# Kernel optimization log

Hardware: AMD Instinct MI355X
Metric: run time of the kernel (lower is better)

The kernel has to match this reference:

```python
import jax, jax.numpy as jnp
import numpy as np

STEPS = 2
P_TOPP = 0.9
TAU = 1.0
LN_EPS = 1e-5


def _top_p_attention(pooled, W1, W2, W3):
    # pooled: (N, C). Bilinear scores -> softmax -> nucleus (top-p) sparsify -> renorm.
    e1 = pooled @ W1.T                      # (N, d)
    e3 = pooled @ W3.T                      # (N, d)
    logits = (e1 @ W2.T) @ e3.T / TAU       # (N, N)
    attn = jax.nn.softmax(logits, axis=-1)
    srt = jnp.sort(attn, axis=-1)[:, ::-1]  # descending
    csum = jnp.cumsum(srt, axis=-1)
    keep = (csum - srt) < P_TOPP            # keep entries whose exclusive cum-prob < p
    thr = jnp.min(jnp.where(keep, srt, jnp.inf), axis=-1, keepdims=True)
    masked = jnp.where(attn >= thr, attn, 0.0)
    return masked / jnp.clip(jnp.sum(masked, axis=-1, keepdims=True), 1e-12)


def _layernorm(h, gamma, beta):
    mu = jnp.mean(h, axis=-1, keepdims=True)
    var = jnp.mean(jnp.square(h - mu), axis=-1, keepdims=True)
    return (h - mu) * jax.lax.rsqrt(var + LN_EPS) * gamma + beta


def _forward(x, prior, W1, W2, W3, prior_fwd_w, adaptive_w, ln_gamma, ln_beta, alpha):
    # Row-normalised prior (forward diffusion operator)
    Rf = prior / jnp.clip(jnp.sum(prior, axis=1, keepdims=True), 1e-12)
    Xf = x
    Xa = x
    residual = jnp.zeros_like(x)
    for idx in range(STEPS):
        pooled = jnp.mean(Xa, axis=1)                      # protein axis pooling -> (N_P, C)
        attn = _top_p_attention(pooled, W1, W2, W3)        # (N_P, N_P)
        Xf = jnp.einsum('ij,jkc->ikc', Rf, Xf)
        Xa = jnp.einsum('ij,jkc->ikc', attn, Xa)
        delta = jnp.einsum('ikc,dc->ikd', Xf, prior_fwd_w[idx]) \
              + jnp.einsum('ikc,dc->ikd', Xa, adaptive_w[idx])
        residual = residual + delta                        # dropout is identity in eval mode
    gate = jax.nn.sigmoid(alpha)                           # (1,)
    return _layernorm(x + gate * residual, ln_gamma, ln_beta)


def setup_inputs() -> dict:
    key = jax.random.key(0)
    ks = jax.random.split(key, 8)
    N_P, N_C, C, D = 2048, 64, 128, 64
    x = jax.random.normal(ks[0], (N_P, N_C, C), dtype=jnp.float32)
    prior = jax.random.uniform(ks[1], (N_P, N_P), dtype=jnp.float32)
    W1 = jax.random.normal(ks[2], (D, C), dtype=jnp.float32) / np.sqrt(C)
    W2 = jax.random.normal(ks[3], (D, D), dtype=jnp.float32) / np.sqrt(D)
    W3 = jax.random.normal(ks[4], (D, C), dtype=jnp.float32) / np.sqrt(C)
    prior_fwd_w = jax.random.normal(ks[5], (STEPS, C, C), dtype=jnp.float32) / np.sqrt(C)
    adaptive_w = jax.random.normal(ks[6], (STEPS, C, C), dtype=jnp.float32) / np.sqrt(C)
    ln_gamma = jnp.ones((C,), dtype=jnp.float32)
    ln_beta = jnp.zeros((C,), dtype=jnp.float32)
    alpha = jnp.zeros((1,), dtype=jnp.float32)
    return {"x": x, "prior": prior, "W1": W1, "W2": W2, "W3": W3,
            "prior_fwd_w": prior_fwd_w, "adaptive_w": adaptive_w,
            "ln_gamma": ln_gamma, "ln_beta": ln_beta, "alpha": alpha}


def reference(x, prior, W1, W2, W3, prior_fwd_w, adaptive_w, ln_gamma, ln_beta, alpha):
    return _forward(x, prior, W1, W2, W3, prior_fwd_w, adaptive_w, ln_gamma, ln_beta, alpha)
```

## Files before the change

kernel.cpp:

```cpp
#include <hip/hip_runtime.h>

typedef unsigned short u16;
typedef __attribute__((ext_vector_type(8))) short short8;
typedef __attribute__((ext_vector_type(4))) float f32x4;
typedef __attribute__((ext_vector_type(16))) float f32x16;

#define AS1 __attribute__((address_space(1)))
#define AS3 __attribute__((address_space(3)))

__device__ __forceinline__ void async_cp16(const void* g, void* l) {
  __builtin_amdgcn_global_load_lds((const AS1 unsigned int*)g, (AS3 unsigned int*)l, 16, 0, 0);
}

__device__ __forceinline__ u16 f2bf(float f) {
  union { float f; unsigned u; } v; v.f = f;
  unsigned r = v.u + 0x7fffu + ((v.u >> 16) & 1u);
  return (u16)(r >> 16);
}
__device__ __forceinline__ float bf2f(u16 h) {
  union { unsigned u; float f; } v; v.u = ((unsigned)h) << 16;
  return v.f;
}

template<int MODE>
__global__ __launch_bounds__(512, 2) void gemm32(
    const u16* __restrict__ A, const u16* __restrict__ B,
    int M, int N, int K,
    u16* __restrict__ Crow, int crow_ld, int crow_coloff,
    u16* __restrict__ Ct, int ct_ld)
{
  extern __shared__ u16 smem[];
  const int tid  = threadIdx.x;
  const int lane = tid & 63;
  const int w    = tid >> 6;
  const int m0 = blockIdx.y * 256;
  const int n0 = blockIdx.x * 256;
  const int wm = w >> 2;
  const int wn = w & 3;
  const int l31  = lane & 31;
  const int half = lane >> 5;
  const int pl   = (l31 & 3) ^ ((l31 >> 2) & 3);

  f32x16 acc[4][2];
#pragma unroll
  for (int i = 0; i < 4; i++)
#pragma unroll
    for (int j = 0; j < 2; j++)
#pragma unroll
      for (int r = 0; r < 16; r++) acc[i][j][r] = 0.f;

  const int sr = lane >> 2;
  const int sc = lane & 3;
  const int rA0 = w * 32 + sr;
  const int rA1 = rA0 + 16;
  const int pA0 = (rA0 & 3) ^ ((rA0 >> 2) & 3);
  const int pA1 = (rA1 & 3) ^ ((rA1 >> 2) & 3);
  const u16* gA0 = A + (size_t)(m0 + rA0) * K + (sc ^ pA0) * 8;
  const u16* gA1 = A + (size_t)(m0 + rA1) * K + (sc ^ pA1) * 8;
  const u16* gB0 = B + (size_t)(n0 + rA0) * K + (sc ^ pA0) * 8;
  const u16* gB1 = B + (size_t)(n0 + rA1) * K + (sc ^ pA1) * 8;
  const int stA0 = (w * 2 + 0) * 512;
  const int stA1 = (w * 2 + 1) * 512;
  const int stB0 = 8192 + stA0;
  const int stB1 = 8192 + stA1;

#define ISSUE(tt) do {                                   \
    u16* sl = smem + ((tt) & 3) * 16384;                 \
    const int ko = (tt) * 32;                            \
    async_cp16(gA0 + ko, sl + stA0);                     \
    async_cp16(gA1 + ko, sl + stA1);                     \
    async_cp16(gB0 + ko, sl + stB0);                     \
    async_cp16(gB1 + ko, sl + stB1);                     \
  } while (0)

  const int NT = K >> 5;
  ISSUE(0); ISSUE(1); ISSUE(2);

  for (int t = 0; t < NT; ++t) {
    const int ahead = NT - 1 - t;
    if (ahead >= 3) {
      ISSUE(t + 3);
      asm volatile("s_waitcnt vmcnt(12)" ::: "memory");
    } else if (ahead == 2) {
      asm volatile("s_waitcnt vmcnt(8)" ::: "memory");
    } else if (ahead == 1) {
      asm volatile("s_waitcnt vmcnt(4)" ::: "memory");
    } else {
      asm volatile("s_waitcnt vmcnt(0)" ::: "memory");
    }
    __builtin_amdgcn_s_barrier();
    asm volatile("" ::: "memory");

    const u16* sAp = smem + (t & 3) * 16384;
    const u16* sBp = sAp + 8192;
#pragma unroll
    for (int ks = 0; ks < 2; ks++) {
      const int kc = ((ks * 2 + half) ^ pl) * 8;
      short8 aF[4], bF[2];
#pragma unroll
      for (int i = 0; i < 4; i++)
        aF[i] = *(const short8*)(sAp + (wm * 128 + i * 32 + l31) * 32 + kc);
#pragma unroll
      for (int j = 0; j < 2; j++)
        bF[j] = *(const short8*)(sBp + (wn * 64 + j * 32 + l31) * 32 + kc);
      __builtin_amdgcn_s_setprio(1);
#pragma unroll
      for (int i = 0; i < 4; i++)
#pragma unroll
        for (int j = 0; j < 2; j++)
          acc[i][j] = __builtin_amdgcn_mfma_f32_32x32x16_bf16(aF[i], bF[j], acc[i][j], 0, 0, 0);
      __builtin_amdgcn_s_setprio(0);
    }

    asm volatile("" ::: "memory");
    __builtin_amdgcn_s_barrier();
    asm volatile("" ::: "memory");
  }
#undef ISSUE

  u16* T = smem;

#pragma unroll
  for (int pr = 0; pr < 4; pr++) {
    if (wm == (pr >> 1)) {
#pragma unroll
      for (int ii = 0; ii < 2; ii++)
#pragma unroll
        for (int j = 0; j < 2; j++)
#pragma unroll
          for (int r = 0; r < 16; r++) {
            const int rloc = ii * 32 + (r & 3) + 8 * (r >> 2) + 4 * half;
            T[rloc * 264 + wn * 64 + j * 32 + l31] = f2bf(acc[(pr & 1) * 2 + ii][j][r]);
          }
    }
    __syncthreads();
    {
      const int row = tid >> 3, c8 = tid & 7;
      const size_t grow = (size_t)(m0 + pr * 64 + row);
      const size_t crow = grow * (size_t)(N >> 7) + (n0 >> 7) + (c8 >> 2);
      u16* dst = Crow + crow * (size_t)crow_ld + crow_coloff + (c8 & 3) * 32;
      const u16* src = T + row * 264 + c8 * 32;
#pragma unroll
      for (int u = 0; u < 4; u++) ((float4*)dst)[u] = ((const float4*)src)[u];
    }
    __syncthreads();
  }

  if constexpr (MODE == 1) {
#pragma unroll
    for (int p = 0; p < 4; p++) {
      if (wn == p) {
#pragma unroll
        for (int i = 0; i < 4; i++)
#pragma unroll
          for (int j = 0; j < 2; j++)
#pragma unroll
            for (int r = 0; r < 16; r++) {
              const int nloc = j * 32 + l31;
              const int mcol = wm * 128 + i * 32 + (r & 3) + 8 * (r >> 2) + 4 * half;
              T[nloc * 264 + mcol] = f2bf(acc[i][j][r]);
            }
      }
      __syncthreads();
      {
        const int row = tid >> 3, c8 = tid & 7;
        u16* dst = Ct + (size_t)(n0 + p * 64 + row) * ct_ld + m0 + c8 * 32;
        const u16* src = T + row * 264 + c8 * 32;
#pragma unroll
        for (int u = 0; u < 4; u++) ((float4*)dst)[u] = ((const float4*)src)[u];
      }
      __syncthreads();
    }
  }
}

template<int MODE>
__global__ __launch_bounds__(256) void gemm_bt(
    const u16* __restrict__ A, const u16* __restrict__ B,
    int M, int N, int K,
    float* __restrict__ Cf,
    u16* __restrict__ Crow, int crow_ld, int crow_coloff)
{
  extern __shared__ char smemc[];
  u16* sA = (u16*)smemc;
  u16* sB = (u16*)(smemc + 8192);
  const int tid  = threadIdx.x;
  const int lane = tid & 63;
  const int wid  = tid >> 6;
  const int m0 = blockIdx.y * 128;
  const int n0 = blockIdx.x * 128;
  const int wm = (wid >> 1) * 64;
  const int wn = (wid & 1) * 64;
  const int ml = lane & 15;
  const int qd = lane >> 4;

  f32x4 acc[4][4];
  const f32x4 zero = {0.f, 0.f, 0.f, 0.f};
#pragma unroll
  for (int i = 0; i < 4; i++)
#pragma unroll
    for (int j = 0; j < 4; j++) acc[i][j] = zero;

  const int r4 = tid >> 2;
  const int c4 = (tid & 3) * 8;
  const u16* gA0 = A + (size_t)(m0 + r4) * K + c4;
  const u16* gA1 = A + (size_t)(m0 + 64 + r4) * K + c4;
  const u16* gB0 = B + (size_t)(n0 + r4) * K + c4;
  const u16* gB1 = B + (size_t)(n0 + 64 + r4) * K + c4;
  u16* lA0 = sA + wid * 512;
  u16* lA1 = sA + 2048 + wid * 512;
  u16* lB0 = sB + wid * 512;
  u16* lB1 = sB + 2048 + wid * 512;

  for (int k0 = 0; k0 < K; k0 += 32) {
    async_cp16(gA0 + k0, lA0);
    async_cp16(gA1 + k0, lA1);
    async_cp16(gB0 + k0, lB0);
    async_cp16(gB1 + k0, lB1);
    __syncthreads();
    short8 af[4], bfr[4];
#pragma unroll
    for (int i = 0; i < 4; i++)
      af[i] = *(const short8*)(sA + (wm + i * 16 + ml) * 32 + qd * 8);
#pragma unroll
    for (int j = 0; j < 4; j++)
      bfr[j] = *(const short8*)(sB + (wn + j * 16 + ml) * 32 + qd * 8);
#pragma unroll
    for (int i = 0; i < 4; i++)
#pragma unroll
      for (int j = 0; j < 4; j++)
        acc[i][j] = __builtin_amdgcn_mfma_f32_16x16x32_bf16(af[i], bfr[j], acc[i][j], 0, 0, 0);
    __syncthreads();
  }

  if constexpr (MODE == 3) {
#pragma unroll
    for (int i = 0; i < 4; i++) {
      const int mr = m0 + wm + i * 16 + qd * 4;
#pragma unroll
      for (int j = 0; j < 4; j++) {
        const int nc = n0 + wn + j * 16 + ml;
        float* p = Cf + (size_t)mr * N + nc;
#pragma unroll
        for (int r = 0; r < 4; r++) p[(size_t)r * N] = acc[i][j][r];
      }
    }
  } else {
    u16* T = (u16*)smemc;
#pragma unroll
    for (int i = 0; i < 4; i++)
#pragma unroll
      for (int j = 0; j < 4; j++)
#pragma unroll
        for (int r = 0; r < 4; r++)
          T[(wm + i * 16 + qd * 4 + r) * 136 + wn + j * 16 + ml] = f2bf(acc[i][j][r]);
    __syncthreads();
    const int row = tid >> 1, halfr = tid & 1;
    const size_t crow = (size_t)(m0 + row) * (N >> 7) + (n0 >> 7);
    u16* dst = Crow + crow * (size_t)crow_ld + crow_coloff + halfr * 64;
    const u16* src = T + row * 136 + halfr * 64;
#pragma unroll
    for (int u = 0; u < 8; u++) ((float4*)dst)[u] = ((const float4*)src)[u];
  }
}

__global__ void rowsum_k(const float* __restrict__ prior, float* __restrict__ rs) {
  const int i = blockIdx.x, t = threadIdx.x;
  const float* p = prior + (size_t)i * 2048;
  float s = 0.f;
  for (int j = t; j < 2048; j += 256) s += p[j];
  __shared__ float red[256];
  red[t] = s; __syncthreads();
  for (int o = 128; o; o >>= 1) { if (t < o) red[t] += red[t + o]; __syncthreads(); }
  if (t == 0) rs[i] = red[0];
}

__global__ void convprior_k(const float4* __restrict__ prior, const float* __restrict__ rs,
                            ushort4* __restrict__ dst) {
  const int idx = blockIdx.x * 256 + threadIdx.x;
  const float inv = 1.0f / rs[idx >> 9];
  const float4 v = prior[idx];
  ushort4 o;
  o.x = f2bf(v.x * inv); o.y = f2bf(v.y * inv); o.z = f2bf(v.z * inv); o.w = f2bf(v.w * inv);
  dst[idx] = o;
}

__global__ void convx_k(const float* __restrict__ x, u16* __restrict__ xt) {
  __shared__ float S[64][65];
  const int t = threadIdx.x;
  const int j0 = blockIdx.y * 64;
  const int n0 = blockIdx.x * 64;
  const int rr = t >> 4, cxc = (t & 15) * 4;
#pragma unroll
  for (int p = 0; p < 4; p++) {
    const float4 v = *(const float4*)(x + (size_t)(j0 + rr + p * 16) * 8192 + n0 + cxc);
    S[rr + p * 16][cxc + 0] = v.x; S[rr + p * 16][cxc + 1] = v.y;
    S[rr + p * 16][cxc + 2] = v.z; S[rr + p * 16][cxc + 3] = v.w;
  }
  __syncthreads();
  const int nl = t >> 2, ch = (t & 3) * 16;
  alignas(16) u16 tmp[16];
#pragma unroll
  for (int u = 0; u < 16; u++) tmp[u] = f2bf(S[ch + u][nl]);
  float4* dst = (float4*)(xt + (size_t)(n0 + nl) * 2048 + j0 + ch);
  dst[0] = ((const float4*)tmp)[0];
  dst[1] = ((const float4*)tmp)[1];
}

__global__ void convw_k(const float* __restrict__ pw, const float* __restrict__ aw,
                        u16* __restrict__ btc) {
  const int idx = blockIdx.x * 256 + threadIdx.x;
  const int k = idx & 255, d = (idx >> 8) & 127, s = idx >> 15;
  const float v = (k < 128) ? aw[(s * 128 + d) * 128 + k] : pw[(s * 128 + d) * 128 + (k - 128)];
  btc[idx] = f2bf(v);
}

__global__ void pooled1_k(const float* __restrict__ x, float* __restrict__ pooled) {
  const int i = blockIdx.x, t = threadIdx.x;
  const int c = t & 127, h = t >> 7;
  const float* base = x + (size_t)i * 8192 + c;
  float s = 0.f;
  for (int k = h * 32; k < h * 32 + 32; k++) s += base[(size_t)k * 128];
  __shared__ float red[256];
  red[t] = s; __syncthreads();
  if (t < 128) pooled[i * 128 + t] = (red[t] + red[t + 128]) * (1.f / 64.f);
}

__global__ void pooled2_k(const u16* __restrict__ comb, float* __restrict__ pooled) {
  const int i = blockIdx.x, t = threadIdx.x;
  const int c = t & 127, h = t >> 7;
  const u16* base = comb + (size_t)i * 64 * 256 + c;
  float s = 0.f;
  for (int k = h * 32; k < h * 32 + 32; k++) s += bf2f(base[(size_t)k * 256]);
  __shared__ float red[256];
  red[t] = s; __syncthreads();
  if (t < 128) pooled[i * 128 + t] = (red[t] + red[t + 128]) * (1.f / 64.f);
}

__global__ void epre_k(const float* __restrict__ pooled,
                       const float* __restrict__ W1, const float* __restrict__ W2,
                       const float* __restrict__ W3,
                       u16* __restrict__ e3b, u16* __restrict__ fb) {
  const int i = blockIdx.x, d = threadIdx.x;
  __shared__ float pr[128], e1s[64];
  pr[d] = pooled[i * 128 + d];
  pr[d + 64] = pooled[i * 128 + 64 + d];
  __syncthreads();
  float s1 = 0.f, s3 = 0.f;
  for (int c = 0; c < 128; c++) {
    const float p = pr[c];
    s1 += p * W1[d * 128 + c];
    s3 += p * W3[d * 128 + c];
  }
  e1s[d] = s1;
  e3b[i * 64 + d] = f2bf(s3);
  __syncthreads();
  float sf = 0.f;
  for (int dd = 0; dd < 64; dd++) sf += e1s[dd] * W2[d * 64 + dd];
  fb[i * 64 + d] = f2bf(sf);
}

__device__ __forceinline__ float waveRedSum(float v) {
#pragma unroll
  for (int o = 1; o < 64; o <<= 1) v += __shfl_xor(v, o);
  return __shfl(v, 0);
}
__device__ __forceinline__ float waveRedMax(float v) {
#pragma unroll
  for (int o = 1; o < 64; o <<= 1) v = fmaxf(v, __shfl_xor(v, o));
  return __shfl(v, 0);
}

__global__ __launch_bounds__(256) void topp_k(const float* __restrict__ logits,
                                              u16* __restrict__ attnb) {
  const int w = threadIdx.x >> 6, l = threadIdx.x & 63;
  const int i = blockIdx.x * 4 + w;
  const float4* row = (const float4*)(logits + (size_t)i * 2048);
  float E[32];
  float mx = -1e30f;
#pragma unroll
  for (int k = 0; k < 8; k++) {
    const float4 v = row[k * 64 + l];
    E[k * 4 + 0] = v.x; E[k * 4 + 1] = v.y; E[k * 4 + 2] = v.z; E[k * 4 + 3] = v.w;
    mx = fmaxf(fmaxf(mx, fmaxf(v.x, v.y)), fmaxf(v.z, v.w));
  }
  mx = waveRedMax(mx);
  float S = 0.f;
#pragma unroll
  for (int u = 0; u < 32; u++) { E[u] = __expf(E[u] - mx); S += E[u]; }
  S = waveRedSum(S);
  const float target = 0.9f * S;
  float lo = 0.f, hi = 1.f;
  for (int it = 0; it < 32; ++it) {
    const float mid = 0.5f * (lo + hi);
    float g = 0.f;
#pragma unroll
    for (int u = 0; u < 32; u++) g += (E[u] > mid) ? E[u] : 0.f;
    g = waveRedSum(g);
    const bool below = (g < target);
    hi = below ? mid : hi;
    lo = below ? lo : mid;
  }
  float Sk = 0.f;
#pragma unroll
  for (int u = 0; u < 32; u++) Sk += (E[u] > lo) ? E[u] : 0.f;
  Sk = waveRedSum(Sk);
  const float inv = 1.f / Sk;
  u16* dst = attnb + (size_t)i * 2048;
#pragma unroll
  for (int k = 0; k < 8; k++) {
    ushort4 o;
    o.x = f2bf(E[k * 4 + 0] > lo ? E[k * 4 + 0] * inv : 0.f);
    o.y = f2bf(E[k * 4 + 1] > lo ? E[k * 4 + 1] * inv : 0.f);
    o.z = f2bf(E[k * 4 + 2] > lo ? E[k * 4 + 2] * inv : 0.f);
    o.w = f2bf(E[k * 4 + 3] > lo ? E[k * 4 + 3] * inv : 0.f);
    *(ushort4*)(dst + k * 256 + l * 4) = o;
  }
}

__global__ void ln_k(const float* __restrict__ x,
                     const u16* __restrict__ d1, const u16* __restrict__ d2,
                     float* __restrict__ out,
                     const float* __restrict__ gamma, const float* __restrict__ beta,
                     const float* __restrict__ alpha) {
  const int wid = threadIdx.x >> 6, lane = threadIdx.x & 63;
  const float gate = 1.f / (1.f + expf(-alpha[0]));
  const float2 g = ((const float2*)gamma)[lane];
  const float2 b = ((const float2*)beta)[lane];
#pragma unroll
  for (int rr = 0; rr < 2; ++rr) {
    const size_t row = (size_t)blockIdx.x * 8 + wid * 2 + rr;
    const float2 xv = ((const float2*)(x + row * 128))[lane];
    const ushort2 r1 = ((const ushort2*)(d1 + row * 128))[lane];
    const ushort2 r2 = ((const ushort2*)(d2 + row * 128))[lane];
    const float h0 = xv.x + gate * (bf2f(r1.x) + bf2f(r2.x));
    const float h1 = xv.y + gate * (bf2f(r1.y) + bf2f(r2.y));
    float s = h0 + h1;
#pragma unroll
    for (int o = 32; o; o >>= 1) s += __shfl_down(s, o);
    const float mu = __shfl(s, 0) * (1.f / 128.f);
    const float d0 = h0 - mu, dd1 = h1 - mu;
    float vs = d0 * d0 + dd1 * dd1;
#pragma unroll
    for (int o = 32; o; o >>= 1) vs += __shfl_down(vs, o);
    const float rstd = rsqrtf(__shfl(vs, 0) * (1.f / 128.f) + 1e-5f);
    float2* op = (float2*)(out + row * 128);
    float2 ov;
    ov.x = d0 * rstd * g.x + b.x;
    ov.y = dd1 * rstd * g.y + b.y;
    op[lane] = ov;
  }
}

extern "C" void kernel_launch(void* const* d_in, const int* in_sizes, int n_in,
                              void* d_out, int out_size, void* d_ws, size_t ws_size,
                              hipStream_t stream) {
  const float* x     = (const float*)d_in[0];
  const float* prior = (const float*)d_in[1];
  const float* W1    = (const float*)d_in[2];
  const float* W2    = (const float*)d_in[3];
  const float* W3    = (const float*)d_in[4];
  const float* Pw    = (const float*)d_in[5];
  const float* Aw    = (const float*)d_in[6];
  const float* gamma = (const float*)d_in[7];
  const float* beta  = (const float*)d_in[8];
  const float* alpha = (const float*)d_in[9];
  float* out = (float*)d_out;

  char* w = (char*)d_ws;
  u16*   Xt_x   = (u16*)(w);
  u16*   XtA    = (u16*)(w + 33554432);
  u16*   XtF    = (u16*)(w + 67108864);
  u16*   comb   = (u16*)(w + 100663296);
  u16*   priorS = (u16*)(w + 167772160);
  u16*   attnb  = (u16*)(w + 176160768);
  float* pooled = (float*)(w + 184549376);
  u16*   e3b    = (u16*)(w + 185597952);
  u16*   fb     = (u16*)(w + 186122240);
  float* rs     = (float*)(w + 186646528);
  u16*   btc    = (u16*)(w + 186654720);
  float* logits1 = (float*)(w + 33554432);
  float* logits2 = (float*)(w);
  u16*   d1      = (u16*)(w);
  u16*   d2      = (u16*)(w + 33554432);
  (void)in_sizes; (void)n_in; (void)ws_size;

  static bool attr_done = false;
  if (!attr_done) {
    hipFuncSetAttribute(reinterpret_cast<const void*>(gemm32<1>),
                        hipFuncAttributeMaxDynamicSharedMemorySize, 131072);
    hipFuncSetAttribute(reinterpret_cast<const void*>(gemm32<2>),
                        hipFuncAttributeMaxDynamicSharedMemorySize, 131072);
    attr_done = true;
  }

  rowsum_k   <<<2048, 256, 0, stream>>>(prior, rs);
  convprior_k<<<4096, 256, 0, stream>>>((const float4*)prior, rs, (ushort4*)priorS);
  convx_k    <<<dim3(128, 32), 256, 0, stream>>>(x, Xt_x);
  convw_k    <<<256, 256, 0, stream>>>(Pw, Aw, btc);

  pooled1_k  <<<2048, 256, 0, stream>>>(x, pooled);
  epre_k     <<<2048, 64, 0, stream>>>(pooled, W1, W2, W3, e3b, fb);
  gemm_bt<3> <<<dim3(16, 16), 256, 16384, stream>>>(fb, e3b, 2048, 2048, 64,
                                                    logits1, nullptr, 0, 0);
  topp_k     <<<512, 256, 0, stream>>>(logits1, attnb);

  gemm32<1><<<dim3(32, 8), 512, 131072, stream>>>(attnb,  Xt_x, 2048, 8192, 2048,
                                                  comb, 256, 0,   XtA, 2048);
  gemm32<1><<<dim3(32, 8), 512, 131072, stream>>>(priorS, Xt_x, 2048, 8192, 2048,
                                                  comb, 256, 128, XtF, 2048);

  pooled2_k  <<<2048, 256, 0, stream>>>(comb, pooled);
  epre_k     <<<2048, 64, 0, stream>>>(pooled, W1, W2, W3, e3b, fb);
  gemm_bt<3> <<<dim3(16, 16), 256, 16384, stream>>>(fb, e3b, 2048, 2048, 64,
                                                    logits2, nullptr, 0, 0);
  topp_k     <<<512, 256, 0, stream>>>(logits2, attnb);

  gemm_bt<2><<<dim3(1, 1024), 256, 34816, stream>>>(comb, btc, 131072, 128, 256,
                                                    nullptr, d1, 128, 0);

  gemm32<2><<<dim3(32, 8), 512, 131072, stream>>>(attnb,  XtA, 2048, 8192, 2048,
                                                  comb, 256, 0,   nullptr, 0);
  gemm32<2><<<dim3(32, 8), 512, 131072, stream>>>(priorS, XtF, 2048, 8192, 2048,
                                                  comb, 256, 128, nullptr, 0);

  gemm_bt<2><<<dim3(1, 1024), 256, 34816, stream>>>(comb, btc + 32768, 131072, 128, 256,
                                                    nullptr, d2, 128, 0);

  ln_k<<<16384, 256, 0, stream>>>(x, d1, d2, out, gamma, beta, alpha);
}
```

Baseline: 663.2 us.

## Restructure GEMM main loop into 8-wave ping-pong schedule with K=64 tiles

Replaces the 4-stage, K=32 async-copy pipeline with a double-buffered K=64 scheme. Each iteration is split into four MFMA quadrants, separated by barriers, with next-tile A/B loads interleaved between them. The LDS swizzle changes to an XOR over 8 chunks to match the 128-byte rows. The aim is better overlap of global loads and LDS reads with MFMA and fewer main-loop iterations, at the cost of more barriers and higher register pressure for the held fragments.

```diff
diff --git a/kernel.cpp b/kernel.cpp
--- a/kernel.cpp
+++ b/kernel.cpp
@@ -39,7 +39,7 @@
   const int wn = w & 3;
   const int l31  = lane & 31;
   const int half = lane >> 5;
-  const int pl   = (l31 & 3) ^ ((l31 >> 2) & 3);
+  const int sw   = l31 & 7;
 
   f32x16 acc[4][2];
 #pragma unroll
@@ -49,74 +49,113 @@
 #pragma unroll
       for (int r = 0; r < 16; r++) acc[i][j][r] = 0.f;
 
-  const int sr = lane >> 2;
-  const int sc = lane & 3;
-  const int rA0 = w * 32 + sr;
-  const int rA1 = rA0 + 16;
-  const int pA0 = (rA0 & 3) ^ ((rA0 >> 2) & 3);
-  const int pA1 = (rA1 & 3) ^ ((rA1 >> 2) & 3);
-  const u16* gA0 = A + (size_t)(m0 + rA0) * K + (sc ^ pA0) * 8;
-  const u16* gA1 = A + (size_t)(m0 + rA1) * K + (sc ^ pA1) * 8;
-  const u16* gB0 = B + (size_t)(n0 + rA0) * K + (sc ^ pA0) * 8;
-  const u16* gB1 = B + (size_t)(n0 + rA1) * K + (sc ^ pA1) * 8;
-  const int stA0 = (w * 2 + 0) * 512;
-  const int stA1 = (w * 2 + 1) * 512;
-  const int stB0 = 8192 + stA0;
-  const int stB1 = 8192 + stA1;
-
-#define ISSUE(tt) do {                                   \
-    u16* sl = smem + ((tt) & 3) * 16384;                 \
-    const int ko = (tt) * 32;                            \
-    async_cp16(gA0 + ko, sl + stA0);                     \
-    async_cp16(gA1 + ko, sl + stA1);                     \
-    async_cp16(gB0 + ko, sl + stB0);                     \
-    async_cp16(gB1 + ko, sl + stB1);                     \
+  const int sub = lane >> 3;
+  const int gch = (lane & 7) ^ sub;
+  const u16* gA0 = A + (size_t)(m0 + w * 32 +  0 + sub) * K + gch * 8;
+  const u16* gA1 = A + (size_t)(m0 + w * 32 +  8 + sub) * K + gch * 8;
+  const u16* gA2 = A + (size_t)(m0 + w * 32 + 16 + sub) * K + gch * 8;
+  const u16* gA3 = A + (size_t)(m0 + w * 32 + 24 + sub) * K + gch * 8;
+  const u16* gB0 = B + (size_t)(n0 + w * 32 +  0 + sub) * K + gch * 8;
+  const u16* gB1 = B + (size_t)(n0 + w * 32 +  8 + sub) * K + gch * 8;
+  const u16* gB2 = B + (size_t)(n0 + w * 32 + 16 + sub) * K + gch * 8;
+  const u16* gB3 = B + (size_t)(n0 + w * 32 + 24 + sub) * K + gch * 8;
+  const int ldsq = w * 4 * 512;
+
+#define ISSUE_A(tt) do {                                         \
+    u16* sl = smem + ((tt) & 1) * 32768 + ldsq;                  \
+    const int ko = (tt) * 64;                                    \
+    async_cp16(gA0 + ko, sl);       async_cp16(gA1 + ko, sl + 512);  \
+    async_cp16(gA2 + ko, sl + 1024); async_cp16(gA3 + ko, sl + 1536);\
   } while (0)
-
-  const int NT = K >> 5;
-  ISSUE(0); ISSUE(1); ISSUE(2);
+#define ISSUE_B(tt) do {                                         \
+    u16* sl = smem + ((tt) & 1) * 32768 + 16384 + ldsq;          \
+    const int ko = (tt) * 64;                                    \
+    async_cp16(gB0 + ko, sl);       async_cp16(gB1 + ko, sl + 512);  \
+    async_cp16(gB2 + ko, sl + 1024); async_cp16(gB3 + ko, sl + 1536);\
+  } while (0)
+
+  const int NT = K >> 6;
+  ISSUE_A(0); ISSUE_B(0);
+  asm volatile("s_waitcnt vmcnt(0)" ::: "memory");
+  __builtin_amdgcn_s_barrier();
 
   for (int t = 0; t < NT; ++t) {
-    const int ahead = NT - 1 - t;
-    if (ahead >= 3) {
-      ISSUE(t + 3);
-      asm volatile("s_waitcnt vmcnt(12)" ::: "memory");
-    } else if (ahead == 2) {
-      asm volatile("s_waitcnt vmcnt(8)" ::: "memory");
-    } else if (ahead == 1) {
-      asm volatile("s_waitcnt vmcnt(4)" ::: "memory");
-    } else {
-      asm volatile("s_waitcnt vmcnt(0)" ::: "memory");
-    }
-    __builtin_amdgcn_s_barrier();
+    const u16* sAp = smem + (t & 1) * 32768;
+    const u16* sBp = sAp + 16384;
+    const bool st = (t + 1 < NT);
+    const int ar = (wm * 128 + l31) * 64;
+    const int br = (wn * 64 + l31) * 64;
+    short8 A01[2][4], A23[2][4], Bj0[4], Bj1[4];
+
+#pragma unroll
+    for (int i = 0; i < 2; i++)
+#pragma unroll
+      for (int ks = 0; ks < 4; ks++)
+        A01[i][ks] = *(const short8*)(sAp + ar + i * 32 * 64 + ((ks * 2 + half) ^ sw) * 8);
+#pragma unroll
+    for (int ks = 0; ks < 4; ks++)
+      Bj0[ks] = *(const short8*)(sBp + br + ((ks * 2 + half) ^ sw) * 8);
+    if (st) ISSUE_A(t + 1);
+    asm volatile("s_waitcnt lgkmcnt(8)" ::: "memory");
+    __builtin_amdgcn_s_barrier();
+    asm volatile("s_waitcnt lgkmcnt(0)" ::: "memory");
+    __builtin_amdgcn_s_setprio(1);
+#pragma unroll
+    for (int i = 0; i < 2; i++)
+#pragma unroll
+      for (int ks = 0; ks < 4; ks++)
+        acc[i][0] = __builtin_amdgcn_mfma_f32_32x32x16_bf16(A01[i][ks], Bj0[ks], acc[i][0], 0, 0, 0);
+    __builtin_amdgcn_s_setprio(0);
     asm volatile("" ::: "memory");
-
-    const u16* sAp = smem + (t & 3) * 16384;
-    const u16* sBp = sAp + 8192;
-#pragma unroll
-    for (int ks = 0; ks < 2; ks++) {
-      const int kc = ((ks * 2 + half) ^ pl) * 8;
-      short8 aF[4], bF[2];
-#pragma unroll
-      for (int i = 0; i < 4; i++)
-        aF[i] = *(const short8*)(sAp + (wm * 128 + i * 32 + l31) * 32 + kc);
-#pragma unroll
-      for (int j = 0; j < 2; j++)
-        bF[j] = *(const short8*)(sBp + (wn * 64 + j * 32 + l31) * 32 + kc);
-      __builtin_amdgcn_s_setprio(1);
-#pragma unroll
-      for (int i = 0; i < 4; i++)
-#pragma unroll
-        for (int j = 0; j < 2; j++)
-          acc[i][j] = __builtin_amdgcn_mfma_f32_32x32x16_bf16(aF[i], bF[j], acc[i][j], 0, 0, 0);
-      __builtin_amdgcn_s_setprio(0);
-    }
-
+    __builtin_amdgcn_s_barrier();
+
+#pragma unroll
+    for (int ks = 0; ks < 4; ks++)
+      Bj1[ks] = *(const short8*)(sBp + br + 32 * 64 + ((ks * 2 + half) ^ sw) * 8);
+    if (st) ISSUE_B(t + 1);
     asm volatile("" ::: "memory");
     __builtin_amdgcn_s_barrier();
+    asm volatile("s_waitcnt lgkmcnt(0)" ::: "memory");
+    __builtin_amdgcn_s_setprio(1);
+#pragma unroll
+    for (int i = 0; i < 2; i++)
+#pragma unroll
+      for (int ks = 0; ks < 4; ks++)
+        acc[i][1] = __builtin_amdgcn_mfma_f32_32x32x16_bf16(A01[i][ks], Bj1[ks], acc[i][1], 0, 0, 0);
+    __builtin_amdgcn_s_setprio(0);
     asm volatile("" ::: "memory");
-  }
-#undef ISSUE
+    __builtin_amdgcn_s_barrier();
+
+#pragma unroll
+    for (int i = 0; i < 2; i++)
+#pragma unroll
+      for (int ks = 0; ks < 4; ks++)
+        A23[i][ks] = *(const short8*)(sAp + ar + (64 + i * 32) * 64 + ((ks * 2 + half) ^ sw) * 8);
+    asm volatile("" ::: "memory");
+    __builtin_amdgcn_s_barrier();
+    asm volatile("s_waitcnt lgkmcnt(0)" ::: "memory");
+    __builtin_amdgcn_s_setprio(1);
+#pragma unroll
+    for (int i = 0; i < 2; i++)
+#pragma unroll
+      for (int ks = 0; ks < 4; ks++)
+        acc[2 + i][1] = __builtin_amdgcn_mfma_f32_32x32x16_bf16(A23[i][ks], Bj1[ks], acc[2 + i][1], 0, 0, 0);
+    __builtin_amdgcn_s_setprio(0);
+    asm volatile("" ::: "memory");
+    __builtin_amdgcn_s_barrier();
+
+    __builtin_amdgcn_s_setprio(1);
+#pragma unroll
+    for (int i = 0; i < 2; i++)
+#pragma unroll
+      for (int ks = 0; ks < 4; ks++)
+        acc[2 + i][0] = __builtin_amdgcn_mfma_f32_32x32x16_bf16(A23[i][ks], Bj0[ks], acc[2 + i][0], 0, 0, 0);
+    __builtin_amdgcn_s_setprio(0);
+    asm volatile("s_waitcnt vmcnt(0)" ::: "memory");
+    __builtin_amdgcn_s_barrier();
+  }
+#undef ISSUE_A
+#undef ISSUE_B
 
   u16* T = smem;
 
```

Measured after the change: 665.0 us. No clear change (+0.3%).
